# Kernel optimization log

Hardware: AMD Instinct MI355X
Metric: run time of the kernel (lower is better)

Reference implementation:

```python
import jax, jax.numpy as jnp
import numpy as np

EPS = 1e-5
NUM_HEADS = 12

def layer_norm(x, g, b):
    mu = jnp.mean(x, axis=-1, keepdims=True)
    var = jnp.var(x, axis=-1, keepdims=True)
    return (x - mu) * jax.lax.rsqrt(var + EPS) * g + b

def setup_inputs() -> dict:
    key = jax.random.key(0)
    ks = jax.random.split(key, 8)
    B, N, Dv, Ds, F = 8, 1024, 768, 512, 768
    def w(k, shape, fan_in):
        return jax.random.normal(k, shape, jnp.float32) * (fan_in ** -0.5)
    return dict(
        visual_features=jax.random.normal(ks[0], (B, N, Dv), jnp.float32),
        semantic_features=jax.random.normal(ks[1], (B, Ds), jnp.float32),
        Wq=w(ks[2], (F, Ds), Ds),
        Wk=w(ks[3], (F, Dv), Dv),
        Wv=w(ks[4], (F, Dv), Dv),
        Wo=w(ks[5], (Dv, F), F),
        bo=jnp.zeros((Dv,), jnp.float32),
        Wg=w(ks[6], (Dv, Dv + Ds), Dv + Ds),
        bg=jnp.zeros((Dv,), jnp.float32),
        gv=jnp.ones((Dv,), jnp.float32),
        bv=jnp.zeros((Dv,), jnp.float32),
        gs=jnp.ones((Ds,), jnp.float32),
        bs=jnp.zeros((Ds,), jnp.float32),
    )

def reference(visual_features, semantic_features, Wq, Wk, Wv, Wo, bo, Wg, bg, gv, bv, gs, bs):
    B, N, Dv = visual_features.shape
    F = Wq.shape[0]
    H = NUM_HEADS
    dh = F // H
    scale = dh ** -0.5
    vis_n = layer_norm(visual_features, gv, bv)           # (B,N,Dv)
    sem_n = layer_norm(semantic_features, gs, bs)         # (B,Ds) — LN over last dim; broadcast-invariant
    # Query is identical for every patch row -> exact single-query collapse of the N x N attention
    q = (sem_n @ Wq.T).reshape(B, H, dh)                  # (B,H,dh)
    k = (vis_n @ Wk.T).reshape(B, N, H, dh).transpose(0, 2, 1, 3)  # (B,H,N,dh)
    v = (vis_n @ Wv.T).reshape(B, N, H, dh).transpose(0, 2, 1, 3)  # (B,H,N,dh)
    scores = jnp.einsum('bhd,bhnd->bhn', q, k) * scale
    attn = jax.nn.softmax(scores, axis=-1)
    ctx = jnp.einsum('bhn,bhnd->bhd', attn, v).reshape(B, F)
    attended = ctx @ Wo.T + bo                            # (B,Dv), same for all N rows (dropout in eval = identity)
    sem_b = jnp.broadcast_to(semantic_features[:, None, :], (B, N, semantic_features.shape[-1]))
    gate_in = jnp.concatenate([visual_features, sem_b], axis=-1)   # (B,N,Dv+Ds)
    gate = jax.nn.sigmoid(gate_in @ Wg.T + bg)            # (B,N,Dv)
    return visual_features + gate * attended[:, None, :]
```

## Files before the change

### kernel.cpp

```cpp
#include <hip/hip_runtime.h>
#include <hip/hip_bf16.h>
#include <math.h>


typedef __attribute__((ext_vector_type(8))) short bf16x8;
typedef __attribute__((ext_vector_type(4))) float f32x4;

#define LN_EPS 1e-5f

__device__ __forceinline__ float bf2f(__hip_bfloat16 h){ return __bfloat162float(h); }

union bfpk8 { uint4 u; __hip_bfloat16 h[8]; };
union bfpk4 { uint2 u; __hip_bfloat16 h[4]; };

__device__ __align__(16) __hip_bfloat16 c_x[8*1024*768];
__device__ __align__(16) __hip_bfloat16 c_sem[8*512];
__device__ __align__(16) __hip_bfloat16 c_Wq[768*512];
__device__ __align__(16) __hip_bfloat16 c_Wk[768*768];
__device__ __align__(16) __hip_bfloat16 c_Wv[768*768];
__device__ __align__(16) __hip_bfloat16 c_Wo[768*768];
__device__ __align__(16) __hip_bfloat16 c_bo[768];
__device__ __align__(16) __hip_bfloat16 c_Wg[768*1280];
__device__ __align__(16) __hip_bfloat16 c_bg[768];
__device__ __align__(16) __hip_bfloat16 c_gv[768];
__device__ __align__(16) __hip_bfloat16 c_bv[768];
__device__ __align__(16) __hip_bfloat16 c_gs[512];
__device__ __align__(16) __hip_bfloat16 c_bs[512];

__device__ __align__(16) __hip_bfloat16 g_gqb[8*16*768];
__device__ __align__(16) float g_A[8*12*768];
__device__ __align__(16) float g_sgq[96];
__device__ __align__(16) float g_bq[96];
__device__ __align__(16) float g_mu[8192];
__device__ __align__(16) float g_rstd[8192];
__device__ __align__(16) float g_w[8*12*1024];
__device__ __align__(16) float g_C[96];
__device__ __align__(16) float g_ctx[8*768];
__device__ __align__(16) float g_att[8*768];
__device__ __align__(16) float g_gsem[8*768];

__device__ __forceinline__ int detect_bf16(const void* gv_raw){
    return ((const unsigned int*)gv_raw)[0] == 0x3F803F80u;
}

__device__ __forceinline__ void conv8(const void* __restrict__ src,
                                      __hip_bfloat16* __restrict__ dst,
                                      int g, int isb){
    if(isb){
        ((uint4*)dst)[g] = ((const uint4*)src)[g];
    } else {
        const float* s = (const float*)src + (size_t)g*8;
        bfpk8 o;
        #pragma unroll
        for(int e=0;e<8;e++) o.h[e] = __float2bfloat16(s[e]);
        ((uint4*)dst)[g] = o.u;
    }
}

#define ING_BLKS 1925
__global__ void k_ingest(const void* s1, const void* s2, const void* s3,
                         const void* s4, const void* s5, const void* s6, const void* s7,
                         const void* s8, const void* s9, const void* s10, const void* s11,
                         const void* s12){
    int i = blockIdx.x*256 + threadIdx.x;
    int isb = detect_bf16(s9);
    if     (i <    512) conv8(s1, c_sem, i,         isb);
    else if(i <  49664) conv8(s2, c_Wq,  i-   512,  isb);
    else if(i < 123392) conv8(s3, c_Wk,  i- 49664,  isb);
    else if(i < 197120) conv8(s4, c_Wv,  i-123392,  isb);
    else if(i < 270848) conv8(s5, c_Wo,  i-197120,  isb);
    else if(i < 270944) conv8(s6, c_bo,  i-270848,  isb);
    else if(i < 393824) conv8(s7, c_Wg,  i-270944,  isb);
    else if(i < 393920) conv8(s8, c_bg,  i-393824,  isb);
    else if(i < 394016) conv8(s9, c_gv,  i-393920,  isb);
    else if(i < 394112) conv8(s10,c_bv,  i-394016,  isb);
    else if(i < 394176) conv8(s11,c_gs,  i-394112,  isb);
    else if(i < 394240) conv8(s12,c_bs,  i-394176,  isb);
    else if(i < 467968) g_A[i-394240]   = 0.f;
    else if(i < 468064) g_sgq[i-467968] = 0.f;
    else if(i < 468160) g_bq[i-468064]  = 0.f;
    else if(i < 474304) g_ctx[i-468160] = 0.f;
    else if(i < 480448) g_att[i-474304] = 0.f;
    else if(i < 492736){
        uint4 z; z.x=0; z.y=0; z.z=0; z.w=0;
        ((uint4*)g_gqb)[i-480448] = z;
    }
}

__global__ __launch_bounds__(256)
void k_qhead(){
    __shared__ float s_semn[8*512];
    __shared__ float s_q2[8][64];
    __shared__ __hip_bfloat16 s_wk[64][64];
    const int t = threadIdx.x, h = blockIdx.y;
    const int c0 = blockIdx.x*64;
    {
        int b = t>>5, l = t&31;
        bfpk8 p0, p1;
        p0.u = *(const uint4*)(c_sem + b*512 + l*16);
        p1.u = *(const uint4*)(c_sem + b*512 + l*16 + 8);
        float v[16], s = 0.f, s2 = 0.f;
        #pragma unroll
        for(int e=0;e<8;e++){ v[e]   = bf2f(p0.h[e]); s += v[e];   s2 += v[e]*v[e]; }
        #pragma unroll
        for(int e=0;e<8;e++){ v[8+e] = bf2f(p1.h[e]); s += v[8+e]; s2 += v[8+e]*v[8+e]; }
        #pragma unroll
        for(int o=16;o>0;o>>=1){ s += __shfl_xor(s,o); s2 += __shfl_xor(s2,o); }
        float mu = s*(1.f/512.f);
        float rstd = rsqrtf(s2*(1.f/512.f) - mu*mu + LN_EPS);
        bfpk8 g0, g1, b0, b1;
        g0.u = *(const uint4*)(c_gs + l*16);   g1.u = *(const uint4*)(c_gs + l*16 + 8);
        b0.u = *(const uint4*)(c_bs + l*16);   b1.u = *(const uint4*)(c_bs + l*16 + 8);
        #pragma unroll
        for(int e=0;e<8;e++){
            s_semn[b*512 + l*16 + e]     = (v[e]-mu)*rstd*bf2f(g0.h[e]) + bf2f(b0.h[e]);
            s_semn[b*512 + l*16 + 8 + e] = (v[8+e]-mu)*rstd*bf2f(g1.h[e]) + bf2f(b1.h[e]);
        }
    }
    for(int i=t;i<512;i+=256){
        int j = i>>3, sl = i&7;
        *(uint4*)(&s_wk[j][sl*8]) = *(const uint4*)(c_Wk + (size_t)(h*64+j)*768 + c0 + sl*8);
    }
    __syncthreads();
    {
        int fi = t & 63, bp = t >> 6;
        int f = h*64 + fi;
        const __hip_bfloat16* wr = c_Wq + (size_t)f*512;
        float a0 = 0.f, a1 = 0.f;
        for(int i0=0;i0<512;i0+=8){
            bfpk8 pk; pk.u = *(const uint4*)(wr + i0);
            #pragma unroll
            for(int c=0;c<8;c++){
                float wv = bf2f(pk.h[c]);
                a0 += wv*s_semn[bp*512 + i0 + c];
                a1 += wv*s_semn[(bp+4)*512 + i0 + c];
            }
        }
        s_q2[bp][fi] = a0; s_q2[bp+4][fi] = a1;
    }
    __syncthreads();
    const int dvl = t & 63, w = t >> 6;
    const int dv = c0 + dvl;
    float a0 = 0.f, a1 = 0.f;
    #pragma unroll 8
    for(int j=0;j<64;j++){
        float wk = bf2f(s_wk[j][dvl]);
        a0 += s_q2[w][j]*wk;
        a1 += s_q2[w+4][j]*wk;
    }
    float gvv = bf2f(c_gv[dv]), bvv = bf2f(c_bv[dv]);
    {
        float g = a0*gvv;
        g_gqb[((size_t)w*16+h)*768 + dv] = __float2bfloat16(g);
        float sg = g, sb = bvv*a0;
        #pragma unroll
        for(int o=32;o>0;o>>=1){ sg += __shfl_xor(sg,o); sb += __shfl_xor(sb,o); }
        if(dvl==0){ atomicAdd(&g_sgq[w*12+h], sg); atomicAdd(&g_bq[w*12+h], sb); }
    }
    {
        float g = a1*gvv;
        g_gqb[((size_t)(w+4)*16+h)*768 + dv] = __float2bfloat16(g);
        float sg = g, sb = bvv*a1;
        #pragma unroll
        for(int o=32;o>0;o>>=1){ sg += __shfl_xor(sg,o); sb += __shfl_xor(sb,o); }
        if(dvl==0){ atomicAdd(&g_sgq[(w+4)*12+h], sg); atomicAdd(&g_bq[(w+4)*12+h], sb); }
    }
}

__global__ __launch_bounds__(256)
void k_gsem(){
    __shared__ float s_sem[8*512];
    __shared__ __hip_bfloat16 s_wg[16*520];
    __shared__ float s_part[128];
    const int t = threadIdx.x;
    const int col0 = blockIdx.x*16;
    for(int i=t;i<512;i+=256){
        bfpk8 p; p.u = *(const uint4*)(c_sem + i*8);
        #pragma unroll
        for(int e=0;e<8;e++) s_sem[i*8+e] = bf2f(p.h[e]);
    }
    for(int i=t;i<16*64;i+=256){
        int rl = i>>6, c = i&63;
        *(uint4*)(s_wg + rl*520 + c*8) =
            *(const uint4*)(c_Wg + (size_t)(col0+rl)*1280 + 768 + c*8);
    }
    __syncthreads();
    const int cl = t&15, bh = t>>4, bb = bh&7, half = bh>>3;
    const __hip_bfloat16* wr = s_wg + cl*520 + half*256;
    const float* sr = s_sem + bb*512 + half*256;
    float a = 0.f;
    for(int k=0;k<256;k+=8){
        bfpk8 p; p.u = *(const uint4*)(wr + k);
        #pragma unroll
        for(int e=0;e<8;e++) a += bf2f(p.h[e])*sr[k+e];
    }
    if(half) s_part[t&127] = a;
    __syncthreads();
    if(!half) g_gsem[bb*768 + col0 + cl] = a + s_part[t&127];
}

__global__ __launch_bounds__(256)
void k_scores(const void* __restrict__ xraw, const void* __restrict__ gvraw){
    __shared__ float s_acc[256*4];
    __shared__ float s_s[4][16], s_s2[4][16];
    __shared__ float s_mu[16], s_rstd[16];
    const int b = blockIdx.y;
    const int t = threadIdx.x, lane = t & 63, w = t >> 6;
    const int isb = detect_bf16(gvraw);
    const int fr = lane & 15, quad = lane >> 4;
    const int n_tile = blockIdx.x*16;
    const size_t row = (size_t)b*1024 + n_tile + fr;
    const __hip_bfloat16* Bp = g_gqb + (size_t)b*16*768 + (size_t)fr*768;
    const int k0 = w*192;

    f32x4 acc = {};
    float s = 0.f, s2 = 0.f;
    if(isb){
        const __hip_bfloat16* xr = (const __hip_bfloat16*)xraw + row*768;
        for(int kb=k0; kb<k0+192; kb+=32){
            bfpk8 pk; pk.u = *(const uint4*)(xr + kb + quad*8);
            *(uint4*)(c_x + row*768 + kb + quad*8) = pk.u;
            #pragma unroll
            for(int e=0;e<8;e++){ float f = bf2f(pk.h[e]); s += f; s2 += f*f; }
            bf16x8 bfrag = *(const bf16x8*)(Bp + kb + quad*8);
            acc = __builtin_amdgcn_mfma_f32_16x16x32_bf16(*(const bf16x8*)&pk, bfrag, acc, 0,0,0);
        }
    } else {
        const float* xr = (const float*)xraw + row*768;
        for(int kb=k0; kb<k0+192; kb+=32){
            f32x4 x0 = *(const f32x4*)(xr + kb + quad*8);
            f32x4 x1 = *(const f32x4*)(xr + kb + quad*8 + 4);
            bfpk8 pk;
            #pragma unroll
            for(int e=0;e<4;e++){ pk.h[e]   = __float2bfloat16(x0[e]); s += x0[e]; s2 += x0[e]*x0[e]; }
            #pragma unroll
            for(int e=0;e<4;e++){ pk.h[4+e] = __float2bfloat16(x1[e]); s += x1[e]; s2 += x1[e]*x1[e]; }
            *(uint4*)(c_x + row*768 + kb + quad*8) = pk.u;
            bf16x8 bfrag = *(const bf16x8*)(Bp + kb + quad*8);
            acc = __builtin_amdgcn_mfma_f32_16x16x32_bf16(*(const bf16x8*)&pk, bfrag, acc, 0,0,0);
        }
    }
    s  += __shfl_xor(s, 16);  s  += __shfl_xor(s, 32);
    s2 += __shfl_xor(s2, 16); s2 += __shfl_xor(s2, 32);
    *(f32x4*)&s_acc[t*4] = acc;
    if(quad == 0){ s_s[w][fr] = s; s_s2[w][fr] = s2; }
    __syncthreads();
    if(w == 0){
        #pragma unroll
        for(int ww=1;ww<4;ww++){
            f32x4 o = *(const f32x4*)&s_acc[(ww*64+lane)*4];
            acc[0]+=o[0]; acc[1]+=o[1]; acc[2]+=o[2]; acc[3]+=o[3];
        }
        if(quad == 0){
            float st  = s_s[0][fr]+s_s[1][fr]+s_s[2][fr]+s_s[3][fr];
            float st2 = s_s2[0][fr]+s_s2[1][fr]+s_s2[2][fr]+s_s2[3][fr];
            float mu = st*(1.f/768.f);
            float rstd = rsqrtf(st2*(1.f/768.f) - mu*mu + LN_EPS);
            g_mu[b*1024 + n_tile + fr] = mu;
            g_rstd[b*1024 + n_tile + fr] = rstd;
            s_mu[fr] = mu; s_rstd[fr] = rstd;
        }
    }
    __syncthreads();
    if(w == 0 && fr < 12){
        float sgqh = g_sgq[b*12+fr];
        float bqh  = g_bq [b*12+fr];
        #pragma unroll
        for(int r=0;r<4;r++){
            int rr = quad*4 + r;
            float val = 0.125f*( s_rstd[rr]*(acc[r] - s_mu[rr]*sgqh) + bqh );
            g_w[((size_t)b*12+fr)*1024 + n_tile + rr] = val;
        }
    }
}

__global__ void k_softmax(){
    int bh = blockIdx.x, b = bh/12, t = threadIdx.x;
    float* sc = g_w + (size_t)bh*1024;
    f32x4 v = *(f32x4*)(sc + t*4);
    float m = fmaxf(fmaxf(v[0],v[1]), fmaxf(v[2],v[3]));
    __shared__ float redm[4], reds[4], redc[4];
    #pragma unroll
    for(int o=32;o>0;o>>=1) m = fmaxf(m, __shfl_xor(m,o));
    if((t&63)==0) redm[t>>6] = m;
    __syncthreads();
    m = fmaxf(fmaxf(redm[0],redm[1]), fmaxf(redm[2],redm[3]));
    float e0=expf(v[0]-m), e1=expf(v[1]-m), e2=expf(v[2]-m), e3=expf(v[3]-m);
    float s = e0+e1+e2+e3;
    #pragma unroll
    for(int o=32;o>0;o>>=1) s += __shfl_xor(s,o);
    if((t&63)==0) reds[t>>6] = s;
    __syncthreads();
    s = reds[0]+reds[1]+reds[2]+reds[3];
    float inv = 1.f/s;
    f32x4 rv = *(f32x4*)(g_rstd + b*1024 + t*4);
    f32x4 mv = *(f32x4*)(g_mu   + b*1024 + t*4);
    f32x4 o4;
    o4[0]=e0*inv*rv[0]; o4[1]=e1*inv*rv[1]; o4[2]=e2*inv*rv[2]; o4[3]=e3*inv*rv[3];
    *(f32x4*)(sc + t*4) = o4;
    float cp = o4[0]*mv[0] + o4[1]*mv[1] + o4[2]*mv[2] + o4[3]*mv[3];
    #pragma unroll
    for(int o=32;o>0;o>>=1) cp += __shfl_xor(cp,o);
    if((t&63)==0) redc[t>>6] = cp;
    __syncthreads();
    if(t==0) g_C[bh] = redc[0]+redc[1]+redc[2]+redc[3];
}

__global__ void k_accA(){
    __shared__ float s_w[12*128];
    int t = threadIdx.x, b = blockIdx.z, n0 = blockIdx.y*128;
    for(int i=t;i<12*128;i+=256){
        int h = i>>7, n = i&127;
        s_w[i] = g_w[((size_t)b*12+h)*1024 + n0 + n];
    }
    __syncthreads();
    int dv = blockIdx.x*256 + t;
    float acc[12] = {0,0,0,0,0,0,0,0,0,0,0,0};
    for(int n=0;n<128;n++){
        float xv = bf2f(c_x[(size_t)(b*1024+n0+n)*768 + dv]);
        #pragma unroll
        for(int h=0;h<12;h++) acc[h] += s_w[h*128+n]*xv;
    }
    #pragma unroll
    for(int h=0;h<12;h++) atomicAdd(&g_A[((size_t)b*12+h)*768 + dv], acc[h]);
}

__global__ void k_ctx(){
    __shared__ float s_wvis[8*68];
    int h = blockIdx.x, ch = blockIdx.y, t = threadIdx.x;
    int base = ch*64;
    {
        int b = t>>6, dvl = t&63;
        int dv = base + dvl;
        s_wvis[b*68+dvl] = bf2f(c_gv[dv])*(g_A[((size_t)b*12+h)*768+dv] - g_C[b*12+h]) + bf2f(c_bv[dv]);
    }
    __syncthreads();
    int f = h*64 + (t>>3), b = t&7;
    const __hip_bfloat16* wr = c_Wv + (size_t)f*768 + base;
    float acc = 0.f;
    #pragma unroll
    for(int d0=0;d0<64;d0+=8){
        bfpk8 pk; pk.u = *(const uint4*)(wr + d0);
        #pragma unroll
        for(int c=0;c<8;c++) acc += s_wvis[b*68 + d0 + c]*bf2f(pk.h[c]);
    }
    atomicAdd(&g_ctx[b*768+f], acc);
}

__global__ void k_att(){
    __shared__ float s_ctx[8*68];
    int ch = blockIdx.y, t = threadIdx.x;
    int base = ch*64;
    {
        int b = t>>6, fl = t&63;
        s_ctx[b*68+fl] = g_ctx[b*768 + base + fl];
    }
    __syncthreads();
    int dv2 = blockIdx.x*64 + (t>>3), b = t&7;
    const __hip_bfloat16* wr = c_Wo + (size_t)dv2*768 + base;
    float acc = (ch==0) ? bf2f(c_bo[dv2]) : 0.f;
    #pragma unroll
    for(int f0=0;f0<64;f0+=8){
        bfpk8 pk; pk.u = *(const uint4*)(wr + f0);
        #pragma unroll
        for(int c=0;c<8;c++) acc += s_ctx[b*68 + f0 + c]*bf2f(pk.h[c]);
    }
    atomicAdd(&g_att[b*768+dv2], acc);
}

__device__ __forceinline__ void stage_gate(int buf, int kb, int m0, int n0,
                                           __hip_bfloat16* As, __hip_bfloat16* Bs,
                                           int wave, int lane){
    const int rl = lane >> 2;
    const int kc = ((lane & 3) ^ ((rl >> 1) & 3))*8;
    #pragma unroll
    for(int s=0;s<2;s++){
        int c = wave + 4*s;
        int row = c*16 + rl;
        const __hip_bfloat16* gp = c_x + (size_t)(m0+row)*768 + kb + kc;
        __builtin_amdgcn_global_load_lds(
            (const __attribute__((address_space(1))) void*)gp,
            (__attribute__((address_space(3))) void*)(As + buf*4096 + c*512),
            16, 0, 0);
    }
    {
        int c = wave;
        int row = c*16 + rl;
        const __hip_bfloat16* gp = c_Wg + (size_t)(n0+row)*1280 + kb + kc;
        __builtin_amdgcn_global_load_lds(
            (const __attribute__((address_space(1))) void*)gp,
            (__attribute__((address_space(3))) void*)(Bs + buf*2048 + c*512),
            16, 0, 0);
    }
}

__global__ __launch_bounds__(256)
void k_gate(void* __restrict__ outv, const void* __restrict__ gv_raw){
    __shared__ __align__(16) __hip_bfloat16 As[4*128*32];
    __shared__ __align__(16) __hip_bfloat16 Bs[4*64*32];
    const int isb = detect_bf16(gv_raw);
    const int t = threadIdx.x;
    const int lin  = blockIdx.y*12 + blockIdx.x;
    const int wgid = (lin & 7)*96 + (lin >> 3);
    const int n0 = (wgid % 12)*64;
    const int m0 = (wgid / 12)*128;
    const int b_blk = m0 >> 10;
    const int lane = t & 63, wave = t >> 6;
    const int wm = (wave>>1)*64, wn = (wave&1)*32;
    const int fr = lane & 15, quad = lane >> 4;
    const int sq = (quad ^ ((fr >> 1) & 3))*8;

    f32x4 acc[4][2] = {};

    stage_gate(0,  0, m0, n0, As, Bs, wave, lane);
    stage_gate(1, 32, m0, n0, As, Bs, wave, lane);
    stage_gate(2, 64, m0, n0, As, Bs, wave, lane);
    for(int it=0; it<24; ++it){
        if(it < 22)       asm volatile("s_waitcnt vmcnt(6)" ::: "memory");
        else if(it == 22) asm volatile("s_waitcnt vmcnt(3)" ::: "memory");
        else              asm volatile("s_waitcnt vmcnt(0)" ::: "memory");
        asm volatile("s_waitcnt lgkmcnt(0)" ::: "memory");
        asm volatile("s_barrier" ::: "memory");
        const __hip_bfloat16* Ab = As + (it&3)*4096;
        const __hip_bfloat16* Bb = Bs + (it&3)*2048;
        bf16x8 af[4], bfr[2];
        #pragma unroll
        for(int i=0;i<4;i++) af[i]  = *(const bf16x8*)(Ab + (wm + i*16 + fr)*32 + sq);
        #pragma unroll
        for(int j=0;j<2;j++) bfr[j] = *(const bf16x8*)(Bb + (wn + j*16 + fr)*32 + sq);
        #pragma unroll
        for(int i=0;i<4;i++)
            #pragma unroll
            for(int j=0;j<2;j++)
                acc[i][j] = __builtin_amdgcn_mfma_f32_16x16x32_bf16(af[i], bfr[j], acc[i][j], 0,0,0);
        if(it < 21)
            stage_gate((it+3)&3, (it+3)*32, m0, n0, As, Bs, wave, lane);
    }

    #pragma unroll
    for(int j=0;j<2;j++){
        int col = n0 + wn + j*16 + fr;
        float attv = g_att[b_blk*768 + col];
        float bgv  = bf2f(c_bg[col]) + g_gsem[b_blk*768 + col];
        #pragma unroll
        for(int i=0;i<4;i++){
            int mbase = m0 + wm + i*16 + quad*4;
            #pragma unroll
            for(int r=0;r<4;r++){
                int m = mbase + r;
                float g = acc[i][j][r] + bgv;
                g = fminf(fmaxf(g, -60.f), 60.f);
                float gate = 1.f/(1.f + expf(-g));
                float xv = bf2f(c_x[(size_t)m*768 + col]);
                float val = xv + gate*attv;
                size_t idx = (size_t)m*768 + col;
                if(isb) ((__hip_bfloat16*)outv)[idx] = __float2bfloat16(val);
                else    ((float*)outv)[idx] = val;
            }
        }
    }
}

extern "C" void kernel_launch(void* const* d_in, const int* in_sizes, int n_in,
                              void* d_out, int out_size, void* d_ws, size_t ws_size,
                              hipStream_t stream){
    (void)in_sizes; (void)n_in; (void)out_size; (void)d_ws; (void)ws_size;

    k_ingest<<<dim3(ING_BLKS), dim3(256), 0, stream>>>(d_in[1], d_in[2], d_in[3],
                                                       d_in[4], d_in[5], d_in[6], d_in[7],
                                                       d_in[8], d_in[9], d_in[10], d_in[11],
                                                       d_in[12]);
    k_qhead<<<dim3(12,12), dim3(256), 0, stream>>>();
    k_gsem<<<dim3(48), dim3(256), 0, stream>>>();
    k_scores<<<dim3(64,8), dim3(256), 0, stream>>>(d_in[0], d_in[9]);
    k_softmax<<<dim3(96), dim3(256), 0, stream>>>();
    k_accA<<<dim3(3,8,8), dim3(256), 0, stream>>>();
    k_ctx<<<dim3(12,12), dim3(512), 0, stream>>>();
    k_att<<<dim3(12,12), dim3(512), 0, stream>>>();
    k_gate<<<dim3(12,64), dim3(256), 0, stream>>>(d_out, d_in[9]);
}
```

Measured before the change: 201.9 us.

## Merge qhead/gsem kernels, fuse softmax into scores via last-block counter, triple-buffer gate

Combines the q-head and semantic-gate precompute kernels into one launch with a block-id split, and folds the softmax into the scores kernel: the last-finishing block per batch (tracked by an atomic counter reset in ingest) performs the softmax for all 12 heads. The gate GEMM pipeline drops from four to three LDS stages with a fully unrolled loop. This removes two kernel launches and their gaps. In exchange the softmax runs serially in one block per batch, and the shallower gate prefetch may hide memory latency less well.

```diff
diff --git a/kernel.cpp b/kernel.cpp
--- a/kernel.cpp
+++ b/kernel.cpp
@@ -38,6 +38,7 @@
 __device__ __align__(16) float g_ctx[8*768];
 __device__ __align__(16) float g_att[8*768];
 __device__ __align__(16) float g_gsem[8*768];
+__device__ unsigned g_done[8];
 
 __device__ __forceinline__ int detect_bf16(const void* gv_raw){
     return ((const unsigned int*)gv_raw)[0] == 0x3F803F80u;
@@ -85,118 +86,121 @@
         uint4 z; z.x=0; z.y=0; z.z=0; z.w=0;
         ((uint4*)g_gqb)[i-480448] = z;
     }
+    else if(i < 492744)
+        __hip_atomic_store(&g_done[i-492736], 0u, __ATOMIC_RELAXED, __HIP_MEMORY_SCOPE_AGENT);
 }
 
 __global__ __launch_bounds__(256)
-void k_qhead(){
-    __shared__ float s_semn[8*512];
-    __shared__ float s_q2[8][64];
-    __shared__ __hip_bfloat16 s_wk[64][64];
-    const int t = threadIdx.x, h = blockIdx.y;
-    const int c0 = blockIdx.x*64;
-    {
-        int b = t>>5, l = t&31;
-        bfpk8 p0, p1;
-        p0.u = *(const uint4*)(c_sem + b*512 + l*16);
-        p1.u = *(const uint4*)(c_sem + b*512 + l*16 + 8);
-        float v[16], s = 0.f, s2 = 0.f;
-        #pragma unroll
-        for(int e=0;e<8;e++){ v[e]   = bf2f(p0.h[e]); s += v[e];   s2 += v[e]*v[e]; }
-        #pragma unroll
-        for(int e=0;e<8;e++){ v[8+e] = bf2f(p1.h[e]); s += v[8+e]; s2 += v[8+e]*v[8+e]; }
-        #pragma unroll
-        for(int o=16;o>0;o>>=1){ s += __shfl_xor(s,o); s2 += __shfl_xor(s2,o); }
-        float mu = s*(1.f/512.f);
-        float rstd = rsqrtf(s2*(1.f/512.f) - mu*mu + LN_EPS);
-        bfpk8 g0, g1, b0, b1;
-        g0.u = *(const uint4*)(c_gs + l*16);   g1.u = *(const uint4*)(c_gs + l*16 + 8);
-        b0.u = *(const uint4*)(c_bs + l*16);   b1.u = *(const uint4*)(c_bs + l*16 + 8);
-        #pragma unroll
-        for(int e=0;e<8;e++){
-            s_semn[b*512 + l*16 + e]     = (v[e]-mu)*rstd*bf2f(g0.h[e]) + bf2f(b0.h[e]);
-            s_semn[b*512 + l*16 + 8 + e] = (v[8+e]-mu)*rstd*bf2f(g1.h[e]) + bf2f(b1.h[e]);
-        }
-    }
-    for(int i=t;i<512;i+=256){
-        int j = i>>3, sl = i&7;
-        *(uint4*)(&s_wk[j][sl*8]) = *(const uint4*)(c_Wk + (size_t)(h*64+j)*768 + c0 + sl*8);
-    }
-    __syncthreads();
-    {
-        int fi = t & 63, bp = t >> 6;
-        int f = h*64 + fi;
-        const __hip_bfloat16* wr = c_Wq + (size_t)f*512;
+void k_pre(){
+    __shared__ __align__(16) unsigned char smem[33536];
+    const int t = threadIdx.x;
+    const int id = blockIdx.x;
+    if(id < 144){
+        float* s_semn = (float*)smem;
+        float* s_q2   = (float*)(smem + 16384);
+        __hip_bfloat16* s_wk = (__hip_bfloat16*)(smem + 18432);
+        const int h = id / 12;
+        const int c0 = (id % 12)*64;
+        {
+            int b = t>>5, l = t&31;
+            bfpk8 p0, p1;
+            p0.u = *(const uint4*)(c_sem + b*512 + l*16);
+            p1.u = *(const uint4*)(c_sem + b*512 + l*16 + 8);
+            float v[16], s = 0.f, s2 = 0.f;
+            #pragma unroll
+            for(int e=0;e<8;e++){ v[e]   = bf2f(p0.h[e]); s += v[e];   s2 += v[e]*v[e]; }
+            #pragma unroll
+            for(int e=0;e<8;e++){ v[8+e] = bf2f(p1.h[e]); s += v[8+e]; s2 += v[8+e]*v[8+e]; }
+            #pragma unroll
+            for(int o=16;o>0;o>>=1){ s += __shfl_xor(s,o); s2 += __shfl_xor(s2,o); }
+            float mu = s*(1.f/512.f);
+            float rstd = rsqrtf(s2*(1.f/512.f) - mu*mu + LN_EPS);
+            bfpk8 g0, g1, b0, b1;
+            g0.u = *(const uint4*)(c_gs + l*16);   g1.u = *(const uint4*)(c_gs + l*16 + 8);
+            b0.u = *(const uint4*)(c_bs + l*16);   b1.u = *(const uint4*)(c_bs + l*16 + 8);
+            #pragma unroll
+            for(int e=0;e<8;e++){
+                s_semn[b*512 + l*16 + e]     = (v[e]-mu)*rstd*bf2f(g0.h[e]) + bf2f(b0.h[e]);
+                s_semn[b*512 + l*16 + 8 + e] = (v[8+e]-mu)*rstd*bf2f(g1.h[e]) + bf2f(b1.h[e]);
+            }
+        }
+        for(int i=t;i<512;i+=256){
+            int j = i>>3, sl = i&7;
+            *(uint4*)(s_wk + j*64 + sl*8) = *(const uint4*)(c_Wk + (size_t)(h*64+j)*768 + c0 + sl*8);
+        }
+        __syncthreads();
+        {
+            int fi = t & 63, bp = t >> 6;
+            int f = h*64 + fi;
+            const __hip_bfloat16* wr = c_Wq + (size_t)f*512;
+            float a0 = 0.f, a1 = 0.f;
+            for(int i0=0;i0<512;i0+=8){
+                bfpk8 pk; pk.u = *(const uint4*)(wr + i0);
+                #pragma unroll
+                for(int c=0;c<8;c++){
+                    float wv = bf2f(pk.h[c]);
+                    a0 += wv*s_semn[bp*512 + i0 + c];
+                    a1 += wv*s_semn[(bp+4)*512 + i0 + c];
+                }
+            }
+            s_q2[bp*64+fi] = a0; s_q2[(bp+4)*64+fi] = a1;
+        }
+        __syncthreads();
+        const int dvl = t & 63, w = t >> 6;
+        const int dv = c0 + dvl;
         float a0 = 0.f, a1 = 0.f;
-        for(int i0=0;i0<512;i0+=8){
-            bfpk8 pk; pk.u = *(const uint4*)(wr + i0);
-            #pragma unroll
-            for(int c=0;c<8;c++){
-                float wv = bf2f(pk.h[c]);
-                a0 += wv*s_semn[bp*512 + i0 + c];
-                a1 += wv*s_semn[(bp+4)*512 + i0 + c];
-            }
-        }
-        s_q2[bp][fi] = a0; s_q2[bp+4][fi] = a1;
-    }
-    __syncthreads();
-    const int dvl = t & 63, w = t >> 6;
-    const int dv = c0 + dvl;
-    float a0 = 0.f, a1 = 0.f;
-    #pragma unroll 8
-    for(int j=0;j<64;j++){
-        float wk = bf2f(s_wk[j][dvl]);
-        a0 += s_q2[w][j]*wk;
-        a1 += s_q2[w+4][j]*wk;
-    }
-    float gvv = bf2f(c_gv[dv]), bvv = bf2f(c_bv[dv]);
-    {
-        float g = a0*gvv;
-        g_gqb[((size_t)w*16+h)*768 + dv] = __float2bfloat16(g);
-        float sg = g, sb = bvv*a0;
-        #pragma unroll
-        for(int o=32;o>0;o>>=1){ sg += __shfl_xor(sg,o); sb += __shfl_xor(sb,o); }
-        if(dvl==0){ atomicAdd(&g_sgq[w*12+h], sg); atomicAdd(&g_bq[w*12+h], sb); }
-    }
-    {
-        float g = a1*gvv;
-        g_gqb[((size_t)(w+4)*16+h)*768 + dv] = __float2bfloat16(g);
-        float sg = g, sb = bvv*a1;
-        #pragma unroll
-        for(int o=32;o>0;o>>=1){ sg += __shfl_xor(sg,o); sb += __shfl_xor(sb,o); }
-        if(dvl==0){ atomicAdd(&g_sgq[(w+4)*12+h], sg); atomicAdd(&g_bq[(w+4)*12+h], sb); }
-    }
-}
-
-__global__ __launch_bounds__(256)
-void k_gsem(){
-    __shared__ float s_sem[8*512];
-    __shared__ __hip_bfloat16 s_wg[16*520];
-    __shared__ float s_part[128];
-    const int t = threadIdx.x;
-    const int col0 = blockIdx.x*16;
-    for(int i=t;i<512;i+=256){
-        bfpk8 p; p.u = *(const uint4*)(c_sem + i*8);
-        #pragma unroll
-        for(int e=0;e<8;e++) s_sem[i*8+e] = bf2f(p.h[e]);
-    }
-    for(int i=t;i<16*64;i+=256){
-        int rl = i>>6, c = i&63;
-        *(uint4*)(s_wg + rl*520 + c*8) =
-            *(const uint4*)(c_Wg + (size_t)(col0+rl)*1280 + 768 + c*8);
-    }
-    __syncthreads();
-    const int cl = t&15, bh = t>>4, bb = bh&7, half = bh>>3;
-    const __hip_bfloat16* wr = s_wg + cl*520 + half*256;
-    const float* sr = s_sem + bb*512 + half*256;
-    float a = 0.f;
-    for(int k=0;k<256;k+=8){
-        bfpk8 p; p.u = *(const uint4*)(wr + k);
-        #pragma unroll
-        for(int e=0;e<8;e++) a += bf2f(p.h[e])*sr[k+e];
-    }
-    if(half) s_part[t&127] = a;
-    __syncthreads();
-    if(!half) g_gsem[bb*768 + col0 + cl] = a + s_part[t&127];
+        #pragma unroll 8
+        for(int j=0;j<64;j++){
+            float wk = bf2f(s_wk[j*64+dvl]);
+            a0 += s_q2[w*64+j]*wk;
+            a1 += s_q2[(w+4)*64+j]*wk;
+        }
+        float gvv = bf2f(c_gv[dv]), bvv = bf2f(c_bv[dv]);
+        {
+            float g = a0*gvv;
+            g_gqb[((size_t)w*16+h)*768 + dv] = __float2bfloat16(g);
+            float sg = g, sb = bvv*a0;
+            #pragma unroll
+            for(int o=32;o>0;o>>=1){ sg += __shfl_xor(sg,o); sb += __shfl_xor(sb,o); }
+            if(dvl==0){ atomicAdd(&g_sgq[w*12+h], sg); atomicAdd(&g_bq[w*12+h], sb); }
+        }
+        {
+            float g = a1*gvv;
+            g_gqb[((size_t)(w+4)*16+h)*768 + dv] = __float2bfloat16(g);
+            float sg = g, sb = bvv*a1;
+            #pragma unroll
+            for(int o=32;o>0;o>>=1){ sg += __shfl_xor(sg,o); sb += __shfl_xor(sb,o); }
+            if(dvl==0){ atomicAdd(&g_sgq[(w+4)*12+h], sg); atomicAdd(&g_bq[(w+4)*12+h], sb); }
+        }
+    } else {
+        float* s_sem = (float*)smem;
+        __hip_bfloat16* s_wg = (__hip_bfloat16*)(smem + 16384);
+        float* s_part = (float*)(smem + 33024);
+        const int col0 = (id - 144)*16;
+        for(int i=t;i<512;i+=256){
+            bfpk8 p; p.u = *(const uint4*)(c_sem + i*8);
+            #pragma unroll
+            for(int e=0;e<8;e++) s_sem[i*8+e] = bf2f(p.h[e]);
+        }
+        for(int i=t;i<16*64;i+=256){
+            int rl = i>>6, c = i&63;
+            *(uint4*)(s_wg + rl*520 + c*8) =
+                *(const uint4*)(c_Wg + (size_t)(col0+rl)*1280 + 768 + c*8);
+        }
+        __syncthreads();
+        const int cl = t&15, bh = t>>4, bb = bh&7, half = bh>>3;
+        const __hip_bfloat16* wr = s_wg + cl*520 + half*256;
+        const float* sr = s_sem + bb*512 + half*256;
+        float a = 0.f;
+        for(int k=0;k<256;k+=8){
+            bfpk8 p; p.u = *(const uint4*)(wr + k);
+            #pragma unroll
+            for(int e=0;e<8;e++) a += bf2f(p.h[e])*sr[k+e];
+        }
+        if(half) s_part[t&127] = a;
+        __syncthreads();
+        if(!half) g_gsem[bb*768 + col0 + cl] = a + s_part[t&127];
+    }
 }
 
 __global__ __launch_bounds__(256)
@@ -204,6 +208,8 @@
     __shared__ float s_acc[256*4];
     __shared__ float s_s[4][16], s_s2[4][16];
     __shared__ float s_mu[16], s_rstd[16];
+    __shared__ float s_red[12];
+    __shared__ unsigned s_lastf;
     const int b = blockIdx.y;
     const int t = threadIdx.x, lane = t & 63, w = t >> 6;
     const int isb = detect_bf16(gvraw);
@@ -256,8 +262,8 @@
             float st2 = s_s2[0][fr]+s_s2[1][fr]+s_s2[2][fr]+s_s2[3][fr];
             float mu = st*(1.f/768.f);
             float rstd = rsqrtf(st2*(1.f/768.f) - mu*mu + LN_EPS);
-            g_mu[b*1024 + n_tile + fr] = mu;
-            g_rstd[b*1024 + n_tile + fr] = rstd;
+            __hip_atomic_store(&g_mu[b*1024 + n_tile + fr],   mu,   __ATOMIC_RELAXED, __HIP_MEMORY_SCOPE_AGENT);
+            __hip_atomic_store(&g_rstd[b*1024 + n_tile + fr], rstd, __ATOMIC_RELAXED, __HIP_MEMORY_SCOPE_AGENT);
             s_mu[fr] = mu; s_rstd[fr] = rstd;
         }
     }
@@ -269,41 +275,56 @@
         for(int r=0;r<4;r++){
             int rr = quad*4 + r;
             float val = 0.125f*( s_rstd[rr]*(acc[r] - s_mu[rr]*sgqh) + bqh );
-            g_w[((size_t)b*12+fr)*1024 + n_tile + rr] = val;
-        }
-    }
-}
-
-__global__ void k_softmax(){
-    int bh = blockIdx.x, b = bh/12, t = threadIdx.x;
-    float* sc = g_w + (size_t)bh*1024;
-    f32x4 v = *(f32x4*)(sc + t*4);
-    float m = fmaxf(fmaxf(v[0],v[1]), fmaxf(v[2],v[3]));
-    __shared__ float redm[4], reds[4], redc[4];
-    #pragma unroll
-    for(int o=32;o>0;o>>=1) m = fmaxf(m, __shfl_xor(m,o));
-    if((t&63)==0) redm[t>>6] = m;
-    __syncthreads();
-    m = fmaxf(fmaxf(redm[0],redm[1]), fmaxf(redm[2],redm[3]));
-    float e0=expf(v[0]-m), e1=expf(v[1]-m), e2=expf(v[2]-m), e3=expf(v[3]-m);
-    float s = e0+e1+e2+e3;
-    #pragma unroll
-    for(int o=32;o>0;o>>=1) s += __shfl_xor(s,o);
-    if((t&63)==0) reds[t>>6] = s;
-    __syncthreads();
-    s = reds[0]+reds[1]+reds[2]+reds[3];
-    float inv = 1.f/s;
-    f32x4 rv = *(f32x4*)(g_rstd + b*1024 + t*4);
-    f32x4 mv = *(f32x4*)(g_mu   + b*1024 + t*4);
-    f32x4 o4;
-    o4[0]=e0*inv*rv[0]; o4[1]=e1*inv*rv[1]; o4[2]=e2*inv*rv[2]; o4[3]=e3*inv*rv[3];
-    *(f32x4*)(sc + t*4) = o4;
-    float cp = o4[0]*mv[0] + o4[1]*mv[1] + o4[2]*mv[2] + o4[3]*mv[3];
-    #pragma unroll
-    for(int o=32;o>0;o>>=1) cp += __shfl_xor(cp,o);
-    if((t&63)==0) redc[t>>6] = cp;
-    __syncthreads();
-    if(t==0) g_C[bh] = redc[0]+redc[1]+redc[2]+redc[3];
+            __hip_atomic_store(&g_w[((size_t)b*12+fr)*1024 + n_tile + rr], val,
+                               __ATOMIC_RELAXED, __HIP_MEMORY_SCOPE_AGENT);
+        }
+    }
+    __syncthreads();
+    if(t == 0){
+        unsigned old = __hip_atomic_fetch_add(&g_done[b], 1u,
+                           __ATOMIC_ACQ_REL, __HIP_MEMORY_SCOPE_AGENT);
+        s_lastf = (old == 63u);
+    }
+    __syncthreads();
+    if(s_lastf){
+        const int n0 = t*4;
+        float mv[4], rv[4];
+        #pragma unroll
+        for(int e=0;e<4;e++){
+            mv[e] = __hip_atomic_load(&g_mu[b*1024+n0+e],   __ATOMIC_RELAXED, __HIP_MEMORY_SCOPE_AGENT);
+            rv[e] = __hip_atomic_load(&g_rstd[b*1024+n0+e], __ATOMIC_RELAXED, __HIP_MEMORY_SCOPE_AGENT);
+        }
+        for(int h=0;h<12;h++){
+            float* sc = g_w + ((size_t)b*12+h)*1024;
+            float v[4];
+            #pragma unroll
+            for(int e=0;e<4;e++)
+                v[e] = __hip_atomic_load(sc+n0+e, __ATOMIC_RELAXED, __HIP_MEMORY_SCOPE_AGENT);
+            float m = fmaxf(fmaxf(v[0],v[1]), fmaxf(v[2],v[3]));
+            #pragma unroll
+            for(int o=32;o>0;o>>=1) m = fmaxf(m, __shfl_xor(m,o));
+            if(lane==0) s_red[w] = m;
+            __syncthreads();
+            m = fmaxf(fmaxf(s_red[0],s_red[1]), fmaxf(s_red[2],s_red[3]));
+            float e0=expf(v[0]-m), e1=expf(v[1]-m), e2=expf(v[2]-m), e3=expf(v[3]-m);
+            float sm = e0+e1+e2+e3;
+            #pragma unroll
+            for(int o=32;o>0;o>>=1) sm += __shfl_xor(sm,o);
+            if(lane==0) s_red[4+w] = sm;
+            __syncthreads();
+            sm = s_red[4]+s_red[5]+s_red[6]+s_red[7];
+            float inv = 1.f/sm;
+            float o0=e0*inv*rv[0], o1=e1*inv*rv[1], o2=e2*inv*rv[2], o3=e3*inv*rv[3];
+            sc[n0]=o0; sc[n0+1]=o1; sc[n0+2]=o2; sc[n0+3]=o3;
+            float cp = o0*mv[0]+o1*mv[1]+o2*mv[2]+o3*mv[3];
+            #pragma unroll
+            for(int o=32;o>0;o>>=1) cp += __shfl_xor(cp,o);
+            if(lane==0) s_red[8+w] = cp;
+            __syncthreads();
+            if(t==0) g_C[b*12+h] = s_red[8]+s_red[9]+s_red[10]+s_red[11];
+            __syncthreads();
+        }
+    }
 }
 
 __global__ void k_accA(){
@@ -396,8 +417,8 @@
 
 __global__ __launch_bounds__(256)
 void k_gate(void* __restrict__ outv, const void* __restrict__ gv_raw){
-    __shared__ __align__(16) __hip_bfloat16 As[4*128*32];
-    __shared__ __align__(16) __hip_bfloat16 Bs[4*64*32];
+    __shared__ __align__(16) __hip_bfloat16 As[3*128*32];
+    __shared__ __align__(16) __hip_bfloat16 Bs[3*64*32];
     const int isb = detect_bf16(gv_raw);
     const int t = threadIdx.x;
     const int lin  = blockIdx.y*12 + blockIdx.x;
@@ -414,15 +435,14 @@
 
     stage_gate(0,  0, m0, n0, As, Bs, wave, lane);
     stage_gate(1, 32, m0, n0, As, Bs, wave, lane);
-    stage_gate(2, 64, m0, n0, As, Bs, wave, lane);
+    #pragma unroll
     for(int it=0; it<24; ++it){
-        if(it < 22)       asm volatile("s_waitcnt vmcnt(6)" ::: "memory");
-        else if(it == 22) asm volatile("s_waitcnt vmcnt(3)" ::: "memory");
-        else              asm volatile("s_waitcnt vmcnt(0)" ::: "memory");
+        if(it < 23) asm volatile("s_waitcnt vmcnt(3)" ::: "memory");
+        else        asm volatile("s_waitcnt vmcnt(0)" ::: "memory");
         asm volatile("s_waitcnt lgkmcnt(0)" ::: "memory");
         asm volatile("s_barrier" ::: "memory");
-        const __hip_bfloat16* Ab = As + (it&3)*4096;
-        const __hip_bfloat16* Bb = Bs + (it&3)*2048;
+        const __hip_bfloat16* Ab = As + (it%3)*4096;
+        const __hip_bfloat16* Bb = Bs + (it%3)*2048;
         bf16x8 af[4], bfr[2];
         #pragma unroll
         for(int i=0;i<4;i++) af[i]  = *(const bf16x8*)(Ab + (wm + i*16 + fr)*32 + sq);
@@ -433,8 +453,8 @@
             #pragma unroll
             for(int j=0;j<2;j++)
                 acc[i][j] = __builtin_amdgcn_mfma_f32_16x16x32_bf16(af[i], bfr[j], acc[i][j], 0,0,0);
-        if(it < 21)
-            stage_gate((it+3)&3, (it+3)*32, m0, n0, As, Bs, wave, lane);
+        if(it < 22)
+            stage_gate((it+2)%3, (it+2)*32, m0, n0, As, Bs, wave, lane);
     }
 
     #pragma unroll
@@ -470,10 +490,8 @@
                                                        d_in[4], d_in[5], d_in[6], d_in[7],
                                                        d_in[8], d_in[9], d_in[10], d_in[11],
                                                        d_in[12]);
-    k_qhead<<<dim3(12,12), dim3(256), 0, stream>>>();
-    k_gsem<<<dim3(48), dim3(256), 0, stream>>>();
+    k_pre<<<dim3(192), dim3(256), 0, stream>>>();
     k_scores<<<dim3(64,8), dim3(256), 0, stream>>>(d_in[0], d_in[9]);
-    k_softmax<<<dim3(96), dim3(256), 0, stream>>>();
     k_accA<<<dim3(3,8,8), dim3(256), 0, stream>>>();
     k_ctx<<<dim3(12,12), dim3(512), 0, stream>>>();
     k_att<<<dim3(12,12), dim3(512), 0, stream>>>();
```

Measured after the change: 232.2 us. 1.15x slower.

## Merge qhead and gsem kernels; shrink gate GEMM pipeline to triple buffering

Applied to the files above, without the earlier changes.

Combines the k_qhead and k_gsem prep kernels into a single k_pre launch that dispatches on block index, removing one kernel launch and its serialization gap. The gate GEMM goes from four to three shared-memory stages with a two-ahead prefetch and a fully unrolled loop, lowering LDS use so more blocks can be resident per CU. In exchange, less load latency is hidden per block, and the modulo-3 buffer indexing depends on unrolling to become constant.

```diff
diff --git a/kernel.cpp b/kernel.cpp
--- a/kernel.cpp
+++ b/kernel.cpp
@@ -88,115 +88,116 @@
 }
 
 __global__ __launch_bounds__(256)
-void k_qhead(){
-    __shared__ float s_semn[8*512];
-    __shared__ float s_q2[8][64];
-    __shared__ __hip_bfloat16 s_wk[64][64];
-    const int t = threadIdx.x, h = blockIdx.y;
-    const int c0 = blockIdx.x*64;
-    {
-        int b = t>>5, l = t&31;
-        bfpk8 p0, p1;
-        p0.u = *(const uint4*)(c_sem + b*512 + l*16);
-        p1.u = *(const uint4*)(c_sem + b*512 + l*16 + 8);
-        float v[16], s = 0.f, s2 = 0.f;
-        #pragma unroll
-        for(int e=0;e<8;e++){ v[e]   = bf2f(p0.h[e]); s += v[e];   s2 += v[e]*v[e]; }
-        #pragma unroll
-        for(int e=0;e<8;e++){ v[8+e] = bf2f(p1.h[e]); s += v[8+e]; s2 += v[8+e]*v[8+e]; }
-        #pragma unroll
-        for(int o=16;o>0;o>>=1){ s += __shfl_xor(s,o); s2 += __shfl_xor(s2,o); }
-        float mu = s*(1.f/512.f);
-        float rstd = rsqrtf(s2*(1.f/512.f) - mu*mu + LN_EPS);
-        bfpk8 g0, g1, b0, b1;
-        g0.u = *(const uint4*)(c_gs + l*16);   g1.u = *(const uint4*)(c_gs + l*16 + 8);
-        b0.u = *(const uint4*)(c_bs + l*16);   b1.u = *(const uint4*)(c_bs + l*16 + 8);
-        #pragma unroll
-        for(int e=0;e<8;e++){
-            s_semn[b*512 + l*16 + e]     = (v[e]-mu)*rstd*bf2f(g0.h[e]) + bf2f(b0.h[e]);
-            s_semn[b*512 + l*16 + 8 + e] = (v[8+e]-mu)*rstd*bf2f(g1.h[e]) + bf2f(b1.h[e]);
-        }
-    }
-    for(int i=t;i<512;i+=256){
-        int j = i>>3, sl = i&7;
-        *(uint4*)(&s_wk[j][sl*8]) = *(const uint4*)(c_Wk + (size_t)(h*64+j)*768 + c0 + sl*8);
-    }
-    __syncthreads();
-    {
-        int fi = t & 63, bp = t >> 6;
-        int f = h*64 + fi;
-        const __hip_bfloat16* wr = c_Wq + (size_t)f*512;
+void k_pre(){
+    __shared__ __align__(16) unsigned char smem[33536];
+    const int t = threadIdx.x;
+    const int id = blockIdx.x;
+    if(id < 144){
+        float* s_semn = (float*)smem;
+        float* s_q2   = (float*)(smem + 16384);
+        __hip_bfloat16* s_wk = (__hip_bfloat16*)(smem + 18432);
+        const int h = id / 12;
+        const int c0 = (id % 12)*64;
+        {
+            int b = t>>5, l = t&31;
+            bfpk8 p0, p1;
+            p0.u = *(const uint4*)(c_sem + b*512 + l*16);
+            p1.u = *(const uint4*)(c_sem + b*512 + l*16 + 8);
+            float v[16], s = 0.f, s2 = 0.f;
+            #pragma unroll
+            for(int e=0;e<8;e++){ v[e]   = bf2f(p0.h[e]); s += v[e];   s2 += v[e]*v[e]; }
+            #pragma unroll
+            for(int e=0;e<8;e++){ v[8+e] = bf2f(p1.h[e]); s += v[8+e]; s2 += v[8+e]*v[8+e]; }
+            #pragma unroll
+            for(int o=16;o>0;o>>=1){ s += __shfl_xor(s,o); s2 += __shfl_xor(s2,o); }
+            float mu = s*(1.f/512.f);
+            float rstd = rsqrtf(s2*(1.f/512.f) - mu*mu + LN_EPS);
+            bfpk8 g0, g1, b0, b1;
+            g0.u = *(const uint4*)(c_gs + l*16);   g1.u = *(const uint4*)(c_gs + l*16 + 8);
+            b0.u = *(const uint4*)(c_bs + l*16);   b1.u = *(const uint4*)(c_bs + l*16 + 8);
+            #pragma unroll
+            for(int e=0;e<8;e++){
+                s_semn[b*512 + l*16 + e]     = (v[e]-mu)*rstd*bf2f(g0.h[e]) + bf2f(b0.h[e]);
+                s_semn[b*512 + l*16 + 8 + e] = (v[8+e]-mu)*rstd*bf2f(g1.h[e]) + bf2f(b1.h[e]);
+            }
+        }
+        for(int i=t;i<512;i+=256){
+            int j = i>>3, sl = i&7;
+            *(uint4*)(s_wk + j*64 + sl*8) = *(const uint4*)(c_Wk + (size_t)(h*64+j)*768 + c0 + sl*8);
+        }
+        __syncthreads();
+        {
+            int fi = t & 63, bp = t >> 6;
+            int f = h*64 + fi;
+            const __hip_bfloat16* wr = c_Wq + (size_t)f*512;
+            float a0 = 0.f, a1 = 0.f;
+            for(int i0=0;i0<512;i0+=8){
+                bfpk8 pk; pk.u = *(const uint4*)(wr + i0);
+                #pragma unroll
+                for(int c=0;c<8;c++){
+                    float wv = bf2f(pk.h[c]);
+                    a0 += wv*s_semn[bp*512 + i0 + c];
+                    a1 += wv*s_semn[(bp+4)*512 + i0 + c];
+                }
+            }
+            s_q2[bp*64+fi] = a0; s_q2[(bp+4)*64+fi] = a1;
+        }
+        __syncthreads();
+        const int dvl = t & 63, w = t >> 6;
+        const int dv = c0 + dvl;
         float a0 = 0.f, a1 = 0.f;
-        for(int i0=0;i0<512;i0+=8){
-            bfpk8 pk; pk.u = *(const uint4*)(wr + i0);
-            #pragma unroll
-            for(int c=0;c<8;c++){
-                float wv = bf2f(pk.h[c]);
-                a0 += wv*s_semn[bp*512 + i0 + c];
-                a1 += wv*s_semn[(bp+4)*512 + i0 + c];
-            }
-        }
-        s_q2[bp][fi] = a0; s_q2[bp+4][fi] = a1;
-    }
-    __syncthreads();
-    const int dvl = t & 63, w = t >> 6;
-    const int dv = c0 + dvl;
-    float a0 = 0.f, a1 = 0.f;
-    #pragma unroll 8
-    for(int j=0;j<64;j++){
-        float wk = bf2f(s_wk[j][dvl]);
-        a0 += s_q2[w][j]*wk;
-        a1 += s_q2[w+4][j]*wk;
-    }
-    float gvv = bf2f(c_gv[dv]), bvv = bf2f(c_bv[dv]);
-    {
-        float g = a0*gvv;
-        g_gqb[((size_t)w*16+h)*768 + dv] = __float2bfloat16(g);
-        float sg = g, sb = bvv*a0;
-        #pragma unroll
-        for(int o=32;o>0;o>>=1){ sg += __shfl_xor(sg,o); sb += __shfl_xor(sb,o); }
-        if(dvl==0){ atomicAdd(&g_sgq[w*12+h], sg); atomicAdd(&g_bq[w*12+h], sb); }
-    }
-    {
-        float g = a1*gvv;
-        g_gqb[((size_t)(w+4)*16+h)*768 + dv] = __float2bfloat16(g);
-        float sg = g, sb = bvv*a1;
-        #pragma unroll
-        for(int o=32;o>0;o>>=1){ sg += __shfl_xor(sg,o); sb += __shfl_xor(sb,o); }
-        if(dvl==0){ atomicAdd(&g_sgq[(w+4)*12+h], sg); atomicAdd(&g_bq[(w+4)*12+h], sb); }
-    }
-}
-
-__global__ __launch_bounds__(256)
-void k_gsem(){
-    __shared__ float s_sem[8*512];
-    __shared__ __hip_bfloat16 s_wg[16*520];
-    __shared__ float s_part[128];
-    const int t = threadIdx.x;
-    const int col0 = blockIdx.x*16;
-    for(int i=t;i<512;i+=256){
-        bfpk8 p; p.u = *(const uint4*)(c_sem + i*8);
-        #pragma unroll
-        for(int e=0;e<8;e++) s_sem[i*8+e] = bf2f(p.h[e]);
-    }
-    for(int i=t;i<16*64;i+=256){
-        int rl = i>>6, c = i&63;
-        *(uint4*)(s_wg + rl*520 + c*8) =
-            *(const uint4*)(c_Wg + (size_t)(col0+rl)*1280 + 768 + c*8);
-    }
-    __syncthreads();
-    const int cl = t&15, bh = t>>4, bb = bh&7, half = bh>>3;
-    const __hip_bfloat16* wr = s_wg + cl*520 + half*256;
-    const float* sr = s_sem + bb*512 + half*256;
-    float a = 0.f;
-    for(int k=0;k<256;k+=8){
-        bfpk8 p; p.u = *(const uint4*)(wr + k);
-        #pragma unroll
-        for(int e=0;e<8;e++) a += bf2f(p.h[e])*sr[k+e];
-    }
-    if(half) s_part[t&127] = a;
-    __syncthreads();
-    if(!half) g_gsem[bb*768 + col0 + cl] = a + s_part[t&127];
+        #pragma unroll 8
+        for(int j=0;j<64;j++){
+            float wk = bf2f(s_wk[j*64+dvl]);
+            a0 += s_q2[w*64+j]*wk;
+            a1 += s_q2[(w+4)*64+j]*wk;
+        }
+        float gvv = bf2f(c_gv[dv]), bvv = bf2f(c_bv[dv]);
+        {
+            float g = a0*gvv;
+            g_gqb[((size_t)w*16+h)*768 + dv] = __float2bfloat16(g);
+            float sg = g, sb = bvv*a0;
+            #pragma unroll
+            for(int o=32;o>0;o>>=1){ sg += __shfl_xor(sg,o); sb += __shfl_xor(sb,o); }
+            if(dvl==0){ atomicAdd(&g_sgq[w*12+h], sg); atomicAdd(&g_bq[w*12+h], sb); }
+        }
+        {
+            float g = a1*gvv;
+            g_gqb[((size_t)(w+4)*16+h)*768 + dv] = __float2bfloat16(g);
+            float sg = g, sb = bvv*a1;
+            #pragma unroll
+            for(int o=32;o>0;o>>=1){ sg += __shfl_xor(sg,o); sb += __shfl_xor(sb,o); }
+            if(dvl==0){ atomicAdd(&g_sgq[(w+4)*12+h], sg); atomicAdd(&g_bq[(w+4)*12+h], sb); }
+        }
+    } else {
+        float* s_sem = (float*)smem;
+        __hip_bfloat16* s_wg = (__hip_bfloat16*)(smem + 16384);
+        float* s_part = (float*)(smem + 33024);
+        const int col0 = (id - 144)*16;
+        for(int i=t;i<512;i+=256){
+            bfpk8 p; p.u = *(const uint4*)(c_sem + i*8);
+            #pragma unroll
+            for(int e=0;e<8;e++) s_sem[i*8+e] = bf2f(p.h[e]);
+        }
+        for(int i=t;i<16*64;i+=256){
+            int rl = i>>6, c = i&63;
+            *(uint4*)(s_wg + rl*520 + c*8) =
+                *(const uint4*)(c_Wg + (size_t)(col0+rl)*1280 + 768 + c*8);
+        }
+        __syncthreads();
+        const int cl = t&15, bh = t>>4, bb = bh&7, half = bh>>3;
+        const __hip_bfloat16* wr = s_wg + cl*520 + half*256;
+        const float* sr = s_sem + bb*512 + half*256;
+        float a = 0.f;
+        for(int k=0;k<256;k+=8){
+            bfpk8 p; p.u = *(const uint4*)(wr + k);
+            #pragma unroll
+            for(int e=0;e<8;e++) a += bf2f(p.h[e])*sr[k+e];
+        }
+        if(half) s_part[t&127] = a;
+        __syncthreads();
+        if(!half) g_gsem[bb*768 + col0 + cl] = a + s_part[t&127];
+    }
 }
 
 __global__ __launch_bounds__(256)
@@ -396,8 +397,8 @@
 
 __global__ __launch_bounds__(256)
 void k_gate(void* __restrict__ outv, const void* __restrict__ gv_raw){
-    __shared__ __align__(16) __hip_bfloat16 As[4*128*32];
-    __shared__ __align__(16) __hip_bfloat16 Bs[4*64*32];
+    __shared__ __align__(16) __hip_bfloat16 As[3*128*32];
+    __shared__ __align__(16) __hip_bfloat16 Bs[3*64*32];
     const int isb = detect_bf16(gv_raw);
     const int t = threadIdx.x;
     const int lin  = blockIdx.y*12 + blockIdx.x;
@@ -414,15 +415,14 @@
 
     stage_gate(0,  0, m0, n0, As, Bs, wave, lane);
     stage_gate(1, 32, m0, n0, As, Bs, wave, lane);
-    stage_gate(2, 64, m0, n0, As, Bs, wave, lane);
+    #pragma unroll
     for(int it=0; it<24; ++it){
-        if(it < 22)       asm volatile("s_waitcnt vmcnt(6)" ::: "memory");
-        else if(it == 22) asm volatile("s_waitcnt vmcnt(3)" ::: "memory");
-        else              asm volatile("s_waitcnt vmcnt(0)" ::: "memory");
+        if(it < 23) asm volatile("s_waitcnt vmcnt(3)" ::: "memory");
+        else        asm volatile("s_waitcnt vmcnt(0)" ::: "memory");
         asm volatile("s_waitcnt lgkmcnt(0)" ::: "memory");
         asm volatile("s_barrier" ::: "memory");
-        const __hip_bfloat16* Ab = As + (it&3)*4096;
-        const __hip_bfloat16* Bb = Bs + (it&3)*2048;
+        const __hip_bfloat16* Ab = As + (it%3)*4096;
+        const __hip_bfloat16* Bb = Bs + (it%3)*2048;
         bf16x8 af[4], bfr[2];
         #pragma unroll
         for(int i=0;i<4;i++) af[i]  = *(const bf16x8*)(Ab + (wm + i*16 + fr)*32 + sq);
@@ -433,8 +433,8 @@
             #pragma unroll
             for(int j=0;j<2;j++)
                 acc[i][j] = __builtin_amdgcn_mfma_f32_16x16x32_bf16(af[i], bfr[j], acc[i][j], 0,0,0);
-        if(it < 21)
-            stage_gate((it+3)&3, (it+3)*32, m0, n0, As, Bs, wave, lane);
+        if(it < 22)
+            stage_gate((it+2)%3, (it+2)*32, m0, n0, As, Bs, wave, lane);
     }
 
     #pragma unroll
@@ -470,8 +470,7 @@
                                                        d_in[4], d_in[5], d_in[6], d_in[7],
                                                        d_in[8], d_in[9], d_in[10], d_in[11],
                                                        d_in[12]);
-    k_qhead<<<dim3(12,12), dim3(256), 0, stream>>>();
-    k_gsem<<<dim3(48), dim3(256), 0, stream>>>();
+    k_pre<<<dim3(192), dim3(256), 0, stream>>>();
     k_scores<<<dim3(64,8), dim3(256), 0, stream>>>(d_in[0], d_in[9]);
     k_softmax<<<dim3(96), dim3(256), 0, stream>>>();
     k_accA<<<dim3(3,8,8), dim3(256), 0, stream>>>();
```

Result: faster. 196.3 us (-2.8%).
